# Kernel tuning notes

Hardware: AMD Instinct MI355X
Metric: run time of the kernel (lower is better)

## Reference

```python
import jax, jax.numpy as jnp
import numpy as np

L, H, C, HS, V, BS = 4, 8, 512, 64, 32000, 2048  # layers, heads, n_embd, head_size, vocab, block_size
B, T = 2, 2048


def _ln(x, g, b, eps=1e-5):
    m = jnp.mean(x, axis=-1, keepdims=True)
    v = jnp.var(x, axis=-1, keepdims=True)
    return (x - m) * jax.lax.rsqrt(v + eps) * g + b


def setup_inputs() -> dict:
    key = jax.random.key(0)
    ks = jax.random.split(key, 12)
    s = 0.02
    f = jnp.float32
    return {
        "idx": jax.random.randint(ks[0], (B, T), 0, V),
        "tok_emb": jax.random.normal(ks[1], (V, C), f) * s,
        "pos_emb": jax.random.normal(ks[2], (BS, C), f) * s,
        "ln1_g": jnp.ones((L, C), f), "ln1_b": jnp.zeros((L, C), f),
        "wq": jax.random.normal(ks[3], (L, H, C, HS), f) * s,
        "wk": jax.random.normal(ks[4], (L, H, C, HS), f) * s,
        "wv": jax.random.normal(ks[5], (L, H, C, HS), f) * s,
        "proj_w": jax.random.normal(ks[6], (L, C, C), f) * s,
        "proj_b": jnp.zeros((L, C), f),
        "ln2_g": jnp.ones((L, C), f), "ln2_b": jnp.zeros((L, C), f),
        "ff_w1": jax.random.normal(ks[7], (L, C, 4 * C), f) * s,
        "ff_b1": jnp.zeros((L, 4 * C), f),
        "ff_w2": jax.random.normal(ks[8], (L, 4 * C, C), f) * s,
        "ff_b2": jnp.zeros((L, C), f),
        "ffln_g": jnp.ones((L, C), f), "ffln_b": jnp.zeros((L, C), f),
        "lm_w": jax.random.normal(ks[9], (C, V), f) * s,
        "lm_b": jnp.zeros((V,), f),
    }


def reference(idx, tok_emb, pos_emb, ln1_g, ln1_b, wq, wk, wv, proj_w, proj_b,
              ln2_g, ln2_b, ff_w1, ff_b1, ff_w2, ff_b2, ffln_g, ffln_b, lm_w, lm_b):
    Tn = idx.shape[1]
    x = tok_emb[idx] + pos_emb[:Tn]  # [B,T,C]
    causal = jnp.tril(jnp.ones((Tn, Tn), bool))
    for l in range(L):
        h = _ln(x, ln1_g[l], ln1_b[l])
        q = jnp.einsum('btc,hcd->bhtd', h, wq[l])
        k = jnp.einsum('btc,hcd->bhtd', h, wk[l])
        v = jnp.einsum('btc,hcd->bhtd', h, wv[l])
        # NOTE: original module does NOT scale by 1/sqrt(head_size)
        wei = jnp.einsum('bhtd,bhsd->bhts', q, k)
        wei = jnp.where(causal, wei, -jnp.inf)
        wei = jax.nn.softmax(wei, axis=-1)
        att = jnp.einsum('bhts,bhsd->bhtd', wei, v)  # [B,H,T,HS]
        att = att.transpose(0, 2, 1, 3).reshape(x.shape[0], Tn, C)
        x = x + att @ proj_w[l].T + proj_b[l]
        h2 = _ln(x, ln2_g[l], ln2_b[l])
        ff = jax.nn.relu(h2 @ ff_w1[l] + ff_b1[l]) @ ff_w2[l] + ff_b2[l]
        ff = _ln(ff, ffln_g[l], ffln_b[l])  # FeedForward has trailing LayerNorm
        x = x + ff
    logits = x @ lm_w + lm_b  # [B,T,V]
    return logits
```

## Files before the change

### kernel.cpp

```cpp
#include <hip/hip_runtime.h>
#include <math.h>

#define NLAYER 4
#define NH     8
#define CDIM   512
#define HS     64
#define VOCAB  32000
#define BB     2
#define TT     2048
#define MROWS  (BB*TT)
#define QKVW   (3*CDIM)
#define NHEADS (BB*NH)
#define ASPLIT 2

typedef __attribute__((ext_vector_type(8))) short bf16x8;
typedef __attribute__((ext_vector_type(4))) float f32x4;

__device__ __forceinline__ unsigned short f2bf(float f) {
    unsigned int u = __float_as_uint(f);
    u += 0x7FFF + ((u >> 16) & 1);
    return (unsigned short)(u >> 16);
}

#define GLOAD16(g, l) __builtin_amdgcn_global_load_lds( \
    (const __attribute__((address_space(1))) void*)(g), \
    (__attribute__((address_space(3))) void*)(l), 16, 0, 0)

#define SWZ(row, chunk) (((row)*64) + ((((chunk) ^ ((row)&7)))*8))

template<int FLAGS, bool OUTBF>
__global__ __launch_bounds__(256) void mfma_gemm(
    const unsigned short* __restrict__ A, int lda,
    const unsigned short* __restrict__ Bt, int ldb,
    const float* __restrict__ bias,
    void* __restrict__ Cout, int ldc,
    const float* __restrict__ resid,
    int K)
{
    __shared__ unsigned short As[2][128*64];
    __shared__ unsigned short Bs[2][128*64];
    const int tid = threadIdx.x;
    const int w = tid >> 6, l = tid & 63;
    const int wr = w >> 1, wc = w & 1;
    const long m0 = (long)blockIdx.y * 128;
    const long n0 = (long)blockIdx.x * 128;
    const int srow = l >> 3;
    const int scol = ((l & 7) ^ (srow & 7)) << 3;
    const unsigned short* Ab = A + m0*lda;
    const unsigned short* Bb = Bt + n0*ldb;
    const int fr = l & 15;
    const int g  = l >> 4;

    f32x4 acc[4][4];
    #pragma unroll
    for (int m = 0; m < 4; m++)
        #pragma unroll
        for (int n = 0; n < 4; n++) acc[m][n] = (f32x4)0.0f;

    auto stage = [&](int k0, int buf) {
        #pragma unroll
        for (int i = 0; i < 4; i++) {
            int seg = w*4 + i;
            GLOAD16(Ab + (long)(seg*8 + srow)*lda + k0 + scol, &As[buf][seg*512]);
            GLOAD16(Bb + (long)(seg*8 + srow)*ldb + k0 + scol, &Bs[buf][seg*512]);
        }
    };

    const int nk = K >> 6;
    stage(0, 0);
    for (int ks = 0; ks < nk; ks++) {
        const int buf = ks & 1;
        __syncthreads();
        if (ks + 1 < nk) stage((ks+1) << 6, buf ^ 1);
        #pragma unroll
        for (int kk = 0; kk < 2; kk++) {
            bf16x8 af[4], bf[4];
            #pragma unroll
            for (int m = 0; m < 4; m++) {
                int row = wr*64 + m*16 + fr;
                af[m] = *(const bf16x8*)&As[buf][SWZ(row, kk*4 + g)];
            }
            #pragma unroll
            for (int n = 0; n < 4; n++) {
                int row = wc*64 + n*16 + fr;
                bf[n] = *(const bf16x8*)&Bs[buf][SWZ(row, kk*4 + g)];
            }
            #pragma unroll
            for (int m = 0; m < 4; m++)
                #pragma unroll
                for (int n = 0; n < 4; n++)
                    acc[m][n] = __builtin_amdgcn_mfma_f32_16x16x32_bf16(
                        af[m], bf[n], acc[m][n], 0, 0, 0);
        }
    }

    const int rg = g << 2;
    #pragma unroll
    for (int n = 0; n < 4; n++) {
        long gn = n0 + wc*64 + n*16 + fr;
        float bv = (FLAGS & 1) ? bias[gn] : 0.f;
        #pragma unroll
        for (int m = 0; m < 4; m++) {
            #pragma unroll
            for (int r = 0; r < 4; r++) {
                long gm = m0 + wr*64 + m*16 + rg + r;
                float val = acc[m][n][r] + bv;
                if (FLAGS & 2) val = fmaxf(val, 0.f);
                if (FLAGS & 4) val += resid[gm*ldc + gn];
                if (OUTBF) ((unsigned short*)Cout)[gm*ldc + gn] = f2bf(val);
                else       ((float*)Cout)[gm*ldc + gn] = val;
            }
        }
    }
}

__global__ __launch_bounds__(512, 2) void mfma_gemm_256(
    const unsigned short* __restrict__ A, int lda,
    const unsigned short* __restrict__ Bt, int ldb,
    const float* __restrict__ bias,
    float* __restrict__ Cout, int ldc,
    int K)
{
    __shared__ unsigned short As[2][256*64];
    __shared__ unsigned short Bs[2][256*64];
    const int tid = threadIdx.x;
    const int w = tid >> 6, l = tid & 63;
    const int wr = w >> 2, wc = w & 3;
    const int mt = gridDim.x;
    const int flat = blockIdx.y * mt + blockIdx.x;
    const int cpx = (mt * gridDim.y) >> 3;
    const int swz = (flat & 7) * cpx + (flat >> 3);
    const long m0 = (long)(swz % mt) * 256;
    const long n0 = (long)(swz / mt) * 256;
    const int srow = l >> 3;
    const int scol = ((l & 7) ^ (srow & 7)) << 3;
    const unsigned short* Ab = A + m0*lda;
    const unsigned short* Bb = Bt + n0*ldb;
    const int fr = l & 15;
    const int g  = l >> 4;

    f32x4 acc[8][4];
    #pragma unroll
    for (int m = 0; m < 8; m++)
        #pragma unroll
        for (int n = 0; n < 4; n++) acc[m][n] = (f32x4)0.0f;

    auto stage = [&](int k0, int buf) {
        #pragma unroll
        for (int i = 0; i < 4; i++) {
            int seg = w*4 + i;
            GLOAD16(Ab + (long)(seg*8 + srow)*lda + k0 + scol, &As[buf][seg*512]);
            GLOAD16(Bb + (long)(seg*8 + srow)*ldb + k0 + scol, &Bs[buf][seg*512]);
        }
    };

    const int nk = K >> 6;
    stage(0, 0);
    for (int ks = 0; ks < nk; ks++) {
        const int buf = ks & 1;
        __syncthreads();
        if (ks + 1 < nk) stage((ks+1) << 6, buf ^ 1);
        #pragma unroll
        for (int kk = 0; kk < 2; kk++) {
            bf16x8 bf[4];
            #pragma unroll
            for (int n = 0; n < 4; n++) {
                int row = wc*64 + n*16 + fr;
                bf[n] = *(const bf16x8*)&Bs[buf][SWZ(row, kk*4 + g)];
            }
            #pragma unroll
            for (int m = 0; m < 8; m++) {
                int row = wr*128 + m*16 + fr;
                bf16x8 af = *(const bf16x8*)&As[buf][SWZ(row, kk*4 + g)];
                #pragma unroll
                for (int n = 0; n < 4; n++)
                    acc[m][n] = __builtin_amdgcn_mfma_f32_16x16x32_bf16(
                        af, bf[n], acc[m][n], 0, 0, 0);
            }
        }
    }

    const int rg = g << 2;
    #pragma unroll
    for (int n = 0; n < 4; n++) {
        long gn = n0 + wc*64 + n*16 + fr;
        float bv = bias[gn];
        #pragma unroll
        for (int m = 0; m < 8; m++) {
            #pragma unroll
            for (int r = 0; r < 4; r++) {
                long gm = m0 + wr*128 + m*16 + rg + r;
                Cout[gm*ldc + gn] = acc[m][n][r] + bv;
            }
        }
    }
}

__global__ __launch_bounds__(256) void mfma_gemm_qkv(
    const unsigned short* __restrict__ A,
    const unsigned short* __restrict__ Bt,
    unsigned short* __restrict__ qh,
    unsigned short* __restrict__ kh,
    unsigned short* __restrict__ vt)
{
    __shared__ unsigned short As[2][128*64];
    __shared__ unsigned short Bs[2][128*64];
    const int tid = threadIdx.x;
    const int w = tid >> 6, l = tid & 63;
    const int wr = w >> 1, wc = w & 1;
    const long m0 = (long)blockIdx.y * 128;
    const long n0 = (long)blockIdx.x * 128;
    const int srow = l >> 3;
    const int scol = ((l & 7) ^ (srow & 7)) << 3;
    const unsigned short* Ab = A + m0*CDIM;
    const unsigned short* Bb = Bt + n0*CDIM;
    const int fr = l & 15;
    const int g  = l >> 4;

    f32x4 acc[4][4];
    #pragma unroll
    for (int m = 0; m < 4; m++)
        #pragma unroll
        for (int n = 0; n < 4; n++) acc[m][n] = (f32x4)0.0f;

    auto stage = [&](int k0, int buf) {
        #pragma unroll
        for (int i = 0; i < 4; i++) {
            int seg = w*4 + i;
            GLOAD16(Ab + (long)(seg*8 + srow)*CDIM + k0 + scol, &As[buf][seg*512]);
            GLOAD16(Bb + (long)(seg*8 + srow)*CDIM + k0 + scol, &Bs[buf][seg*512]);
        }
    };

    const int nk = CDIM >> 6;
    stage(0, 0);
    for (int ks = 0; ks < nk; ks++) {
        const int buf = ks & 1;
        __syncthreads();
        if (ks + 1 < nk) stage((ks+1) << 6, buf ^ 1);
        #pragma unroll
        for (int kk = 0; kk < 2; kk++) {
            bf16x8 af[4], bf[4];
            #pragma unroll
            for (int m = 0; m < 4; m++) {
                int row = wr*64 + m*16 + fr;
                af[m] = *(const bf16x8*)&As[buf][SWZ(row, kk*4 + g)];
            }
            #pragma unroll
            for (int n = 0; n < 4; n++) {
                int row = wc*64 + n*16 + fr;
                bf[n] = *(const bf16x8*)&Bs[buf][SWZ(row, kk*4 + g)];
            }
            #pragma unroll
            for (int m = 0; m < 4; m++)
                #pragma unroll
                for (int n = 0; n < 4; n++)
                    acc[m][n] = __builtin_amdgcn_mfma_f32_16x16x32_bf16(
                        af[m], bf[n], acc[m][n], 0, 0, 0);
        }
    }

    const int rg = g << 2;
    #pragma unroll
    for (int n = 0; n < 4; n++) {
        int gn = (int)(n0 + wc*64 + n*16 + fr);
        int which = gn >> 9, hh = (gn >> 6) & 7, d = gn & 63;
        #pragma unroll
        for (int m = 0; m < 4; m++) {
            #pragma unroll
            for (int r = 0; r < 4; r++) {
                int gm = (int)(m0 + wr*64 + m*16 + rg + r);
                int b = gm >> 11, t = gm & (TT-1);
                int head = b*NH + hh;
                unsigned short val = f2bf(acc[m][n][r]);
                if (which == 0)      qh[((long)head*TT + t)*HS + d] = val;
                else if (which == 1) kh[((long)head*TT + t)*HS + d] = val;
                else                 vt[((long)head*HS + d)*TT + t] = val;
            }
        }
    }
}

__global__ __launch_bounds__(256) void attn_part(
    const unsigned short* __restrict__ qh,
    const unsigned short* __restrict__ kh,
    const unsigned short* __restrict__ vt,
    float* __restrict__ oP, float* __restrict__ ml)
{
    __shared__ unsigned short Ks[2][64*64];
    __shared__ unsigned short Vts[2][64*64];
    __shared__ unsigned short Ps[4][32*72];
    const int tid = threadIdx.x;
    const int w = tid >> 6, l = tid & 63;
    const int fr = l & 15, g = l >> 4;
    const int head = blockIdx.y;
    const int sp = blockIdx.z;
    const int x = blockIdx.x;
    const int qw = x*128 + w*32;
    const unsigned short* Qb = qh + (long)head*TT*HS;
    const unsigned short* Kb = kh + (long)head*TT*HS;
    const unsigned short* Vb = vt + (long)head*HS*TT;

    bf16x8 aq[2][2];
    #pragma unroll
    for (int mt = 0; mt < 2; mt++)
        #pragma unroll
        for (int ks = 0; ks < 2; ks++)
            aq[mt][ks] = *(const bf16x8*)&Qb[(long)(qw + mt*16 + fr)*HS + ks*32 + g*8];

    f32x4 acc_o[2][4];
    float mrun[2][4], lsum[2][4];
    #pragma unroll
    for (int mt = 0; mt < 2; mt++) {
        #pragma unroll
        for (int r = 0; r < 4; r++) { mrun[mt][r] = -INFINITY; lsum[mt][r] = 0.f; }
        #pragma unroll
        for (int n = 0; n < 4; n++) acc_o[mt][n] = (f32x4)0.0f;
    }

    const int nch = 2*x + 2;
    const int qq = nch / ASPLIT, rr = nch % ASPLIT;
    const int cbeg = sp*qq + (sp < rr ? sp : rr);
    const int cend = cbeg + qq + (sp < rr ? 1 : 0);
    const int srow = l >> 3;
    const int scol = ((l & 7) ^ (srow & 7)) << 3;

    auto stage = [&](int c) {
        int buf = c & 1;
        int s0_ = c*64;
        #pragma unroll
        for (int i = 0; i < 2; i++) {
            int rb = i*32 + w*8;
            GLOAD16(Kb + (long)(s0_ + rb + srow)*HS + scol, &Ks[buf][rb*64]);
            GLOAD16(Vb + (long)(rb + srow)*TT + s0_ + scol, &Vts[buf][rb*64]);
        }
    };

    if (cbeg < cend) stage(cbeg);
    for (int c = cbeg; c < cend; c++) {
        const int s0 = c*64;
        const int buf = c & 1;
        __syncthreads();
        if (c + 1 < cend) stage(c+1);
        if (s0 > qw + 31) continue;

        bf16x8 bk[4][2];
        #pragma unroll
        for (int n = 0; n < 4; n++)
            #pragma unroll
            for (int ks = 0; ks < 2; ks++) {
                int row = n*16 + fr;
                bk[n][ks] = *(const bf16x8*)&Ks[buf][SWZ(row, ks*4 + g)];
            }
        f32x4 sc[2][4];
        #pragma unroll
        for (int mt = 0; mt < 2; mt++)
            #pragma unroll
            for (int n = 0; n < 4; n++) sc[mt][n] = (f32x4)0.0f;
        #pragma unroll
        for (int ks = 0; ks < 2; ks++)
            #pragma unroll
            for (int mt = 0; mt < 2; mt++)
                #pragma unroll
                for (int n = 0; n < 4; n++)
                    sc[mt][n] = __builtin_amdgcn_mfma_f32_16x16x32_bf16(
                        aq[mt][ks], bk[n][ks], sc[mt][n], 0, 0, 0);

        #pragma unroll
        for (int mt = 0; mt < 2; mt++) {
            #pragma unroll
            for (int r = 0; r < 4; r++) {
                int q = qw + mt*16 + g*4 + r;
                float rmax = -INFINITY;
                #pragma unroll
                for (int n = 0; n < 4; n++) {
                    float v = sc[mt][n][r];
                    v = (s0 + n*16 + fr <= q) ? v : -INFINITY;
                    sc[mt][n][r] = v;
                    rmax = fmaxf(rmax, v);
                }
                #pragma unroll
                for (int off = 8; off >= 1; off >>= 1)
                    rmax = fmaxf(rmax, __shfl_xor(rmax, off));
                float mnew = fmaxf(mrun[mt][r], rmax);
                float scale = __expf(mrun[mt][r] - mnew);
                float ps = 0.f;
                #pragma unroll
                for (int n = 0; n < 4; n++) {
                    float p = __expf(sc[mt][n][r] - mnew);
                    sc[mt][n][r] = p;
                    ps += p;
                }
                #pragma unroll
                for (int off = 8; off >= 1; off >>= 1)
                    ps += __shfl_xor(ps, off);
                lsum[mt][r] = lsum[mt][r]*scale + ps;
                mrun[mt][r] = mnew;
                #pragma unroll
                for (int n = 0; n < 4; n++) acc_o[mt][n][r] *= scale;
            }
        }

        #pragma unroll
        for (int mt = 0; mt < 2; mt++)
            #pragma unroll
            for (int n = 0; n < 4; n++)
                #pragma unroll
                for (int r = 0; r < 4; r++)
                    Ps[w][(mt*16 + g*4 + r)*72 + n*16 + fr] = f2bf(sc[mt][n][r]);

        bf16x8 ap[2][2], bv[4][2];
        #pragma unroll
        for (int mt = 0; mt < 2; mt++)
            #pragma unroll
            for (int ks = 0; ks < 2; ks++)
                ap[mt][ks] = *(const bf16x8*)&Ps[w][(mt*16 + fr)*72 + ks*32 + g*8];
        #pragma unroll
        for (int n = 0; n < 4; n++)
            #pragma unroll
            for (int ks = 0; ks < 2; ks++) {
                int row = n*16 + fr;
                bv[n][ks] = *(const bf16x8*)&Vts[buf][SWZ(row, ks*4 + g)];
            }
        #pragma unroll
        for (int ks = 0; ks < 2; ks++)
            #pragma unroll
            for (int mt = 0; mt < 2; mt++)
                #pragma unroll
                for (int n = 0; n < 4; n++)
                    acc_o[mt][n] = __builtin_amdgcn_mfma_f32_16x16x32_bf16(
                        ap[mt][ks], bv[n][ks], acc_o[mt][n], 0, 0, 0);
    }

    float* oB = oP + ((long)(head*ASPLIT + sp)*TT)*HS;
    float* mlB = ml + ((long)(head*ASPLIT + sp)*TT)*2;
    #pragma unroll
    for (int mt = 0; mt < 2; mt++) {
        #pragma unroll
        for (int n = 0; n < 4; n++)
            #pragma unroll
            for (int r = 0; r < 4; r++)
                oB[(long)(qw + mt*16 + g*4 + r)*HS + n*16 + fr] = acc_o[mt][n][r];
        if (fr == 0) {
            #pragma unroll
            for (int r = 0; r < 4; r++) {
                int t = qw + mt*16 + g*4 + r;
                mlB[t*2]     = mrun[mt][r];
                mlB[t*2 + 1] = lsum[mt][r];
            }
        }
    }
}

__global__ __launch_bounds__(256) void attn_combine(
    const float* __restrict__ oP, const float* __restrict__ ml,
    unsigned short* __restrict__ att)
{
    const int gid = blockIdx.x*4 + (threadIdx.x >> 6);
    const int lane = threadIdx.x & 63;
    const int head = gid >> 11, t = gid & (TT-1);
    const int b = head >> 3, hh = head & 7;
    float m[ASPLIT], lv[ASPLIT];
    float M = -INFINITY;
    #pragma unroll
    for (int s = 0; s < ASPLIT; s++) {
        long i = (long)(head*ASPLIT + s)*TT + t;
        m[s] = ml[i*2]; lv[s] = ml[i*2+1];
        M = fmaxf(M, m[s]);
    }
    float L = 0.f, v = 0.f;
    #pragma unroll
    for (int s = 0; s < ASPLIT; s++) {
        float e = __expf(m[s] - M);
        L += lv[s]*e;
        v += oP[((long)(head*ASPLIT + s)*TT + t)*HS + lane]*e;
    }
    att[((long)b*TT + t)*CDIM + hh*HS + lane] = f2bf(v / L);
}

__global__ __launch_bounds__(256) void transpose_cast(
    const float* __restrict__ in, unsigned short* __restrict__ out,
    int R, int Cn, long in_z1, long in_z2, long out_z1, long out_z2, int z2n)
{
    const int z = blockIdx.z;
    const int z1 = z / z2n, z2 = z % z2n;
    const float* ip = in + (long)z1*in_z1 + (long)z2*in_z2;
    unsigned short* op = out + (long)z1*out_z1 + (long)z2*out_z2;
    __shared__ float tile[32][33];
    const int tx = threadIdx.x & 31, ty = threadIdx.x >> 5;
    const long r0 = (long)blockIdx.y*32, c0 = (long)blockIdx.x*32;
    #pragma unroll
    for (int i = 0; i < 4; i++)
        tile[ty + i*8][tx] = ip[(r0 + ty + i*8)*Cn + c0 + tx];
    __syncthreads();
    #pragma unroll
    for (int i = 0; i < 4; i++)
        op[(c0 + ty + i*8)*R + r0 + tx] = f2bf(tile[tx][ty + i*8]);
}

__global__ __launch_bounds__(256) void cast_kernel(
    const float* __restrict__ in, unsigned short* __restrict__ out, long n)
{
    long i = ((long)blockIdx.x*256 + threadIdx.x) * 4;
    if (i >= n) return;
    float4 v = *(const float4*)(in + i);
    ushort4 u = make_ushort4(f2bf(v.x), f2bf(v.y), f2bf(v.z), f2bf(v.w));
    *(ushort4*)(out + i) = u;
}

__global__ void embed_kernel(const int* __restrict__ idx,
                             const float* __restrict__ tok,
                             const float* __restrict__ pos,
                             float* __restrict__ x)
{
    const int r = blockIdx.x;
    const int t = r & (TT-1);
    const long tr = idx[r];
    const float* te = tok + tr*CDIM;
    const float* pe = pos + (long)t*CDIM;
    float* xo = x + (long)r*CDIM;
    for (int c = threadIdx.x; c < CDIM; c += blockDim.x)
        xo[c] = te[c] + pe[c];
}

template<int MODE>
__global__ __launch_bounds__(256) void ln_kernel(
    const float* __restrict__ in, const float* __restrict__ g,
    const float* __restrict__ bb, void* __restrict__ outp,
    void* __restrict__ outp2)
{
    const int wave = threadIdx.x >> 6;
    const int lane = threadIdx.x & 63;
    const long r = (long)blockIdx.x*4 + wave;
    const float* xr = in + r*CDIM;
    float vals[8];
    float s = 0.f;
    #pragma unroll
    for (int i = 0; i < 8; i++) { vals[i] = xr[lane + i*64]; s += vals[i]; }
    #pragma unroll
    for (int o = 32; o >= 1; o >>= 1) s += __shfl_xor(s, o);
    const float mean = s * (1.f/CDIM);
    float vs = 0.f;
    #pragma unroll
    for (int i = 0; i < 8; i++) { float d = vals[i]-mean; vs += d*d; }
    #pragma unroll
    for (int o = 32; o >= 1; o >>= 1) vs += __shfl_xor(vs, o);
    const float rstd = rsqrtf(vs*(1.f/CDIM) + 1e-5f);
    #pragma unroll
    for (int i = 0; i < 8; i++) {
        int c = lane + i*64;
        float nv = (vals[i]-mean)*rstd*g[c] + bb[c];
        if (MODE == 1) {
            ((unsigned short*)outp)[r*CDIM + c] = f2bf(nv);
        } else {
            float s2 = ((float*)outp)[r*CDIM + c] + nv;
            ((float*)outp)[r*CDIM + c] = s2;
            if (MODE == 3) ((unsigned short*)outp2)[r*CDIM + c] = f2bf(s2);
        }
    }
}

extern "C" void kernel_launch(void* const* d_in, const int* in_sizes, int n_in,
                              void* d_out, int out_size, void* d_ws, size_t ws_size,
                              hipStream_t stream)
{
    const int*   idx   = (const int*)  d_in[0];
    const float* tok   = (const float*)d_in[1];
    const float* pos   = (const float*)d_in[2];
    const float* ln1g  = (const float*)d_in[3];
    const float* ln1b  = (const float*)d_in[4];
    const float* wq    = (const float*)d_in[5];
    const float* wk    = (const float*)d_in[6];
    const float* wv    = (const float*)d_in[7];
    const float* projw = (const float*)d_in[8];
    const float* projb = (const float*)d_in[9];
    const float* ln2g  = (const float*)d_in[10];
    const float* ln2b  = (const float*)d_in[11];
    const float* ffw1  = (const float*)d_in[12];
    const float* ffb1  = (const float*)d_in[13];
    const float* ffw2  = (const float*)d_in[14];
    const float* ffb2  = (const float*)d_in[15];
    const float* flng  = (const float*)d_in[16];
    const float* flnb  = (const float*)d_in[17];
    const float* lmw   = (const float*)d_in[18];
    const float* lmb   = (const float*)d_in[19];
    float* out = (float*)d_out;

    char* wp = (char*)d_ws;
    float* x  = (float*)wp;           wp += (size_t)MROWS*CDIM*4;
    float* ff = (float*)wp;           wp += (size_t)MROWS*CDIM*4;
    unsigned short* h     = (unsigned short*)wp; wp += (size_t)MROWS*CDIM*2;
    unsigned short* lmt   = (unsigned short*)wp; wp += (size_t)VOCAB*CDIM*2;
    unsigned short* ff1t  = (unsigned short*)wp; wp += (size_t)NLAYER*4*CDIM*CDIM*2;
    unsigned short* ff2t  = (unsigned short*)wp; wp += (size_t)NLAYER*4*CDIM*CDIM*2;
    unsigned short* qkvt  = (unsigned short*)wp; wp += (size_t)NLAYER*QKVW*CDIM*2;
    unsigned short* projc = (unsigned short*)wp; wp += (size_t)NLAYER*CDIM*CDIM*2;
    unsigned short* qh    = (unsigned short*)wp; wp += (size_t)NHEADS*TT*HS*2;
    unsigned short* kh    = (unsigned short*)wp; wp += (size_t)NHEADS*TT*HS*2;
    unsigned short* vt    = (unsigned short*)wp; wp += (size_t)NHEADS*TT*HS*2;

    unsigned short* f1  = (unsigned short*)d_out;
    unsigned short* att = f1 + (size_t)MROWS*4*CDIM;
    float* oP = (float*)(att + (size_t)MROWS*CDIM);
    float* ml = oP + (size_t)NHEADS*ASPLIT*TT*HS;

    transpose_cast<<<dim3(VOCAB/32, CDIM/32, 1), 256, 0, stream>>>(
        lmw, lmt, CDIM, VOCAB, 0, 0, 0, 0, 1);
    transpose_cast<<<dim3(4*CDIM/32, CDIM/32, NLAYER), 256, 0, stream>>>(
        ffw1, ff1t, CDIM, 4*CDIM, (long)CDIM*4*CDIM, 0, (long)4*CDIM*CDIM, 0, 1);
    transpose_cast<<<dim3(CDIM/32, 4*CDIM/32, NLAYER), 256, 0, stream>>>(
        ffw2, ff2t, 4*CDIM, CDIM, (long)4*CDIM*CDIM, 0, (long)CDIM*4*CDIM, 0, 1);
    {
        const size_t QBLK = (size_t)CDIM * CDIM;
        transpose_cast<<<dim3(HS/32, CDIM/32, NLAYER*NH), 256, 0, stream>>>(
            wq, qkvt,            CDIM, HS,
            (long)NH*CDIM*HS, (long)CDIM*HS, (long)QKVW*CDIM, (long)HS*CDIM, NH);
        transpose_cast<<<dim3(HS/32, CDIM/32, NLAYER*NH), 256, 0, stream>>>(
            wk, qkvt + QBLK,     CDIM, HS,
            (long)NH*CDIM*HS, (long)CDIM*HS, (long)QKVW*CDIM, (long)HS*CDIM, NH);
        transpose_cast<<<dim3(HS/32, CDIM/32, NLAYER*NH), 256, 0, stream>>>(
            wv, qkvt + 2*QBLK,   CDIM, HS,
            (long)NH*CDIM*HS, (long)CDIM*HS, (long)QKVW*CDIM, (long)HS*CDIM, NH);
    }
    cast_kernel<<<(NLAYER*CDIM*CDIM/4 + 255)/256, 256, 0, stream>>>(
        projw, projc, (long)NLAYER*CDIM*CDIM);

    embed_kernel<<<MROWS, 256, 0, stream>>>(idx, tok, pos, x);

    for (int l = 0; l < NLAYER; l++) {
        const unsigned short* qkvt_l = qkvt + (size_t)l*QKVW*CDIM;
        const unsigned short* projc_l = projc + (size_t)l*CDIM*CDIM;
        const unsigned short* ff1t_l = ff1t + (size_t)l*4*CDIM*CDIM;
        const unsigned short* ff2t_l = ff2t + (size_t)l*4*CDIM*CDIM;

        ln_kernel<1><<<MROWS/4, 256, 0, stream>>>(x, ln1g + l*CDIM, ln1b + l*CDIM, h, nullptr);

        mfma_gemm_qkv<<<dim3(QKVW/128, MROWS/128), 256, 0, stream>>>(
            h, qkvt_l, qh, kh, vt);

        attn_part<<<dim3(TT/128, NHEADS, ASPLIT), 256, 0, stream>>>(qh, kh, vt, oP, ml);
        attn_combine<<<dim3(NHEADS*TT/4), 256, 0, stream>>>(oP, ml, att);

        mfma_gemm<5,false><<<dim3(CDIM/128, MROWS/128), 256, 0, stream>>>(
            att, CDIM, projc_l, CDIM, projb + l*CDIM, x, CDIM, x, CDIM);

        ln_kernel<1><<<MROWS/4, 256, 0, stream>>>(x, ln2g + l*CDIM, ln2b + l*CDIM, h, nullptr);

        mfma_gemm<3,true><<<dim3(4*CDIM/128, MROWS/128), 256, 0, stream>>>(
            h, CDIM, ff1t_l, CDIM, ffb1 + (size_t)l*4*CDIM, f1, 4*CDIM, nullptr, CDIM);

        mfma_gemm<1,false><<<dim3(CDIM/128, MROWS/128), 256, 0, stream>>>(
            f1, 4*CDIM, ff2t_l, 4*CDIM, ffb2 + l*CDIM, ff, CDIM, nullptr, 4*CDIM);

        if (l == NLAYER-1)
            ln_kernel<3><<<MROWS/4, 256, 0, stream>>>(ff, flng + l*CDIM, flnb + l*CDIM, x, h);
        else
            ln_kernel<2><<<MROWS/4, 256, 0, stream>>>(ff, flng + l*CDIM, flnb + l*CDIM, x, nullptr);
    }

    mfma_gemm_256<<<dim3(MROWS/256, VOCAB/256), 512, 0, stream>>>(
        h, CDIM, lmt, CDIM, lmb, out, VOCAB, CDIM);
}
```

Baseline: 1.002 ms.

## Keep full A tile resident in LDS for LM head, stream B from registers

```diff
diff --git a/kernel.cpp b/kernel.cpp
--- a/kernel.cpp
+++ b/kernel.cpp
@@ -114,84 +114,91 @@
     }
 }
 
-__global__ __launch_bounds__(512, 2) void mfma_gemm_256(
-    const unsigned short* __restrict__ A, int lda,
-    const unsigned short* __restrict__ Bt, int ldb,
+__global__ __launch_bounds__(256) void lmhead_gemm(
+    const unsigned short* __restrict__ A,
+    const unsigned short* __restrict__ Bt,
     const float* __restrict__ bias,
-    float* __restrict__ Cout, int ldc,
-    int K)
-{
-    __shared__ unsigned short As[2][256*64];
-    __shared__ unsigned short Bs[2][256*64];
+    float* __restrict__ Cout)
+{
+    __shared__ unsigned short Afull[8][128*64];
     const int tid = threadIdx.x;
     const int w = tid >> 6, l = tid & 63;
-    const int wr = w >> 2, wc = w & 3;
-    const int mt = gridDim.x;
-    const int flat = blockIdx.y * mt + blockIdx.x;
-    const int cpx = (mt * gridDim.y) >> 3;
-    const int swz = (flat & 7) * cpx + (flat >> 3);
-    const long m0 = (long)(swz % mt) * 256;
-    const long n0 = (long)(swz / mt) * 256;
+    const int wr = w >> 1, wc = w & 1;
+    const int fr = l & 15, g = l >> 4;
     const int srow = l >> 3;
     const int scol = ((l & 7) ^ (srow & 7)) << 3;
-    const unsigned short* Ab = A + m0*lda;
-    const unsigned short* Bb = Bt + n0*ldb;
-    const int fr = l & 15;
-    const int g  = l >> 4;
-
-    f32x4 acc[8][4];
-    #pragma unroll
-    for (int m = 0; m < 8; m++)
-        #pragma unroll
-        for (int n = 0; n < 4; n++) acc[m][n] = (f32x4)0.0f;
-
-    auto stage = [&](int k0, int buf) {
+    const int mtile = blockIdx.y;
+    const int ng = blockIdx.x;
+    const long m0 = (long)mtile * 128;
+
+    #pragma unroll
+    for (int ks = 0; ks < 8; ks++)
         #pragma unroll
         for (int i = 0; i < 4; i++) {
             int seg = w*4 + i;
-            GLOAD16(Ab + (long)(seg*8 + srow)*lda + k0 + scol, &As[buf][seg*512]);
-            GLOAD16(Bb + (long)(seg*8 + srow)*ldb + k0 + scol, &Bs[buf][seg*512]);
-        }
+            GLOAD16(A + (long)(m0 + seg*8 + srow)*CDIM + ks*64 + scol,
+                    &Afull[ks][seg*512]);
+        }
+
+    const int q = 250/8, r = 250%8;
+    const int nbeg = ng*q + (ng < r ? ng : r);
+    const int nend = nbeg + q + (ng < r ? 1 : 0);
+
+    bf16x8 bfn[4][2];
+    auto loadB = [&](bf16x8 (&dst)[4][2], int nt, int ks) {
+        const unsigned short* Bb = Bt + (long)nt*128*CDIM;
+        #pragma unroll
+        for (int n = 0; n < 4; n++)
+            #pragma unroll
+            for (int kk = 0; kk < 2; kk++)
+                dst[n][kk] = *(const bf16x8*)&Bb[(long)(wc*64 + n*16 + fr)*CDIM
+                                                 + ks*64 + kk*32 + g*8];
     };
-
-    const int nk = K >> 6;
-    stage(0, 0);
-    for (int ks = 0; ks < nk; ks++) {
-        const int buf = ks & 1;
-        __syncthreads();
-        if (ks + 1 < nk) stage((ks+1) << 6, buf ^ 1);
-        #pragma unroll
-        for (int kk = 0; kk < 2; kk++) {
-            bf16x8 bf[4];
-            #pragma unroll
-            for (int n = 0; n < 4; n++) {
-                int row = wc*64 + n*16 + fr;
-                bf[n] = *(const bf16x8*)&Bs[buf][SWZ(row, kk*4 + g)];
-            }
-            #pragma unroll
-            for (int m = 0; m < 8; m++) {
-                int row = wr*128 + m*16 + fr;
-                bf16x8 af = *(const bf16x8*)&As[buf][SWZ(row, kk*4 + g)];
-                #pragma unroll
-                for (int n = 0; n < 4; n++)
-                    acc[m][n] = __builtin_amdgcn_mfma_f32_16x16x32_bf16(
-                        af, bf[n], acc[m][n], 0, 0, 0);
-            }
-        }
-    }
-
-    const int rg = g << 2;
-    #pragma unroll
-    for (int n = 0; n < 4; n++) {
-        long gn = n0 + wc*64 + n*16 + fr;
-        float bv = bias[gn];
-        #pragma unroll
-        for (int m = 0; m < 8; m++) {
-            #pragma unroll
-            for (int r = 0; r < 4; r++) {
-                long gm = m0 + wr*128 + m*16 + rg + r;
-                Cout[gm*ldc + gn] = acc[m][n][r] + bv;
-            }
+    loadB(bfn, nbeg, 0);
+    __syncthreads();
+
+    for (int nt = nbeg; nt < nend; nt++) {
+        f32x4 acc[4][4];
+        #pragma unroll
+        for (int m = 0; m < 4; m++)
+            #pragma unroll
+            for (int n = 0; n < 4; n++) acc[m][n] = (f32x4)0.0f;
+
+        #pragma unroll
+        for (int ks = 0; ks < 8; ks++) {
+            bf16x8 bfc[4][2];
+            #pragma unroll
+            for (int n = 0; n < 4; n++)
+                #pragma unroll
+                for (int kk = 0; kk < 2; kk++) bfc[n][kk] = bfn[n][kk];
+            if (ks < 7)             loadB(bfn, nt, ks+1);
+            else if (nt + 1 < nend) loadB(bfn, nt+1, 0);
+            #pragma unroll
+            for (int kk = 0; kk < 2; kk++)
+                #pragma unroll
+                for (int m = 0; m < 4; m++) {
+                    int row = wr*64 + m*16 + fr;
+                    bf16x8 af = *(const bf16x8*)&Afull[ks][SWZ(row, kk*4 + g)];
+                    #pragma unroll
+                    for (int n = 0; n < 4; n++)
+                        acc[m][n] = __builtin_amdgcn_mfma_f32_16x16x32_bf16(
+                            af, bfc[n][kk], acc[m][n], 0, 0, 0);
+                }
+        }
+
+        const int rg = g << 2;
+        const long n0 = (long)nt * 128;
+        #pragma unroll
+        for (int n = 0; n < 4; n++) {
+            long gn = n0 + wc*64 + n*16 + fr;
+            float bv = bias[gn];
+            #pragma unroll
+            for (int m = 0; m < 4; m++)
+                #pragma unroll
+                for (int rr = 0; rr < 4; rr++) {
+                    long gm = m0 + wr*64 + m*16 + rg + rr;
+                    Cout[gm*VOCAB + gn] = acc[m][n][rr] + bv;
+                }
         }
     }
 }
@@ -658,6 +665,5 @@
             ln_kernel<2><<<MROWS/4, 256, 0, stream>>>(ff, flng + l*CDIM, flnb + l*CDIM, x, nullptr);
     }
 
-    mfma_gemm_256<<<dim3(MROWS/256, VOCAB/256), 512, 0, stream>>>(
-        h, CDIM, lmt, CDIM, lmb, out, VOCAB, CDIM);
-}
+    lmhead_gemm<<<dim3(8, 32), 256, 0, stream>>>(h, lmt, lmb, out);
+}
```

Result: slower. 1.227 ms (+22.5%).

## Replace 256x256 double-buffered LM-head GEMM with single-buffered 128x128 tiles

Applied to the files above, without the earlier changes.

```diff
diff --git a/kernel.cpp b/kernel.cpp
--- a/kernel.cpp
+++ b/kernel.cpp
@@ -114,69 +114,64 @@
     }
 }
 
-__global__ __launch_bounds__(512, 2) void mfma_gemm_256(
-    const unsigned short* __restrict__ A, int lda,
-    const unsigned short* __restrict__ Bt, int ldb,
+__global__ __launch_bounds__(256) void mfma_gemm_lm(
+    const unsigned short* __restrict__ A,
+    const unsigned short* __restrict__ Bt,
     const float* __restrict__ bias,
-    float* __restrict__ Cout, int ldc,
-    int K)
-{
-    __shared__ unsigned short As[2][256*64];
-    __shared__ unsigned short Bs[2][256*64];
+    float* __restrict__ Cout)
+{
+    __shared__ unsigned short As[128*64];
+    __shared__ unsigned short Bs[128*64];
     const int tid = threadIdx.x;
     const int w = tid >> 6, l = tid & 63;
-    const int wr = w >> 2, wc = w & 3;
+    const int wr = w >> 1, wc = w & 1;
     const int mt = gridDim.x;
     const int flat = blockIdx.y * mt + blockIdx.x;
     const int cpx = (mt * gridDim.y) >> 3;
     const int swz = (flat & 7) * cpx + (flat >> 3);
-    const long m0 = (long)(swz % mt) * 256;
-    const long n0 = (long)(swz / mt) * 256;
+    const long m0 = (long)(swz % mt) * 128;
+    const long n0 = (long)(swz / mt) * 128;
     const int srow = l >> 3;
     const int scol = ((l & 7) ^ (srow & 7)) << 3;
-    const unsigned short* Ab = A + m0*lda;
-    const unsigned short* Bb = Bt + n0*ldb;
+    const unsigned short* Ab = A + m0*CDIM;
+    const unsigned short* Bb = Bt + n0*CDIM;
     const int fr = l & 15;
     const int g  = l >> 4;
 
-    f32x4 acc[8][4];
-    #pragma unroll
-    for (int m = 0; m < 8; m++)
+    f32x4 acc[4][4];
+    #pragma unroll
+    for (int m = 0; m < 4; m++)
         #pragma unroll
         for (int n = 0; n < 4; n++) acc[m][n] = (f32x4)0.0f;
 
-    auto stage = [&](int k0, int buf) {
+    for (int k0 = 0; k0 < CDIM; k0 += 64) {
+        __syncthreads();
         #pragma unroll
         for (int i = 0; i < 4; i++) {
             int seg = w*4 + i;
-            GLOAD16(Ab + (long)(seg*8 + srow)*lda + k0 + scol, &As[buf][seg*512]);
-            GLOAD16(Bb + (long)(seg*8 + srow)*ldb + k0 + scol, &Bs[buf][seg*512]);
-        }
-    };
-
-    const int nk = K >> 6;
-    stage(0, 0);
-    for (int ks = 0; ks < nk; ks++) {
-        const int buf = ks & 1;
+            GLOAD16(Ab + (long)(seg*8 + srow)*CDIM + k0 + scol, As + seg*512);
+            GLOAD16(Bb + (long)(seg*8 + srow)*CDIM + k0 + scol, Bs + seg*512);
+        }
         __syncthreads();
-        if (ks + 1 < nk) stage((ks+1) << 6, buf ^ 1);
         #pragma unroll
         for (int kk = 0; kk < 2; kk++) {
-            bf16x8 bf[4];
+            bf16x8 af[4], bf[4];
+            #pragma unroll
+            for (int m = 0; m < 4; m++) {
+                int row = wr*64 + m*16 + fr;
+                af[m] = *(const bf16x8*)&As[SWZ(row, kk*4 + g)];
+            }
             #pragma unroll
             for (int n = 0; n < 4; n++) {
                 int row = wc*64 + n*16 + fr;
-                bf[n] = *(const bf16x8*)&Bs[buf][SWZ(row, kk*4 + g)];
-            }
-            #pragma unroll
-            for (int m = 0; m < 8; m++) {
-                int row = wr*128 + m*16 + fr;
-                bf16x8 af = *(const bf16x8*)&As[buf][SWZ(row, kk*4 + g)];
+                bf[n] = *(const bf16x8*)&Bs[SWZ(row, kk*4 + g)];
+            }
+            #pragma unroll
+            for (int m = 0; m < 4; m++)
                 #pragma unroll
                 for (int n = 0; n < 4; n++)
                     acc[m][n] = __builtin_amdgcn_mfma_f32_16x16x32_bf16(
-                        af, bf[n], acc[m][n], 0, 0, 0);
-            }
+                        af[m], bf[n], acc[m][n], 0, 0, 0);
         }
     }
 
@@ -186,13 +181,12 @@
         long gn = n0 + wc*64 + n*16 + fr;
         float bv = bias[gn];
         #pragma unroll
-        for (int m = 0; m < 8; m++) {
+        for (int m = 0; m < 4; m++)
             #pragma unroll
             for (int r = 0; r < 4; r++) {
-                long gm = m0 + wr*128 + m*16 + rg + r;
-                Cout[gm*ldc + gn] = acc[m][n][r] + bv;
-            }
-        }
+                long gm = m0 + wr*64 + m*16 + rg + r;
+                Cout[gm*VOCAB + gn] = acc[m][n][r] + bv;
+            }
     }
 }
 
@@ -658,6 +652,5 @@
             ln_kernel<2><<<MROWS/4, 256, 0, stream>>>(ff, flng + l*CDIM, flnb + l*CDIM, x, nullptr);
     }
 
-    mfma_gemm_256<<<dim3(MROWS/256, VOCAB/256), 512, 0, stream>>>(
-        h, CDIM, lmt, CDIM, lmb, out, VOCAB, CDIM);
-}
+    mfma_gemm_lm<<<dim3(MROWS/128, VOCAB/128), 256, 0, stream>>>(h, lmt, lmb, out);
+}
```

New measurement: 1.048 ms. 4.6% more time.
